# Kernel tuning notes

Measured on AMD Instinct MI355X. Metric: run time of the kernel, lower is better.

Reference implementation:

```python
import jax, jax.numpy as jnp
import numpy as np

EMBED = 1024
B, S = 4, 2048

def setup_inputs() -> dict:
    key = jax.random.key(0)
    k1, k2, k3, k4, k5, k6 = jax.random.split(key, 6)
    scale = 1.0 / np.sqrt(EMBED)
    return {
        "query": jax.random.normal(k1, (B, S, EMBED), dtype=jnp.float32),
        "key": jax.random.normal(k2, (B, S, EMBED), dtype=jnp.float32),
        "value": jax.random.normal(k3, (B, S, EMBED), dtype=jnp.float32),
        # nn.Linear weights, stored torch-style [out, in]; y = x @ W.T
        "Q_W": jax.random.normal(k4, (EMBED, EMBED), dtype=jnp.float32) * scale,
        "K_W": jax.random.normal(k5, (EMBED, EMBED), dtype=jnp.float32) * scale,
        "V_W": jax.random.normal(k6, (EMBED, EMBED), dtype=jnp.float32) * scale,
    }

def reference(query, key, value, Q_W, K_W, V_W):
    q = jnp.einsum('bse,oe->bso', query, Q_W)   # Linear(bias=False): x @ W.T
    k = jnp.einsum('bse,oe->bso', key, K_W)
    v = jnp.einsum('bse,oe->bso', value, V_W)
    scores = jnp.einsum('bqe,bke->bqk', q, k) / jnp.sqrt(jnp.asarray(q.shape[-1], q.dtype))
    attn = jax.nn.softmax(scores, axis=-1)      # [b, q, k]
    out = jnp.einsum('bqs,bse->bqe', attn, v)
    return out
```

## Files before the change

### kernel.cpp

```cpp
#include <hip/hip_runtime.h>
#include <stdint.h>


typedef __attribute__((ext_vector_type(8))) short short8;
typedef __attribute__((ext_vector_type(4))) float floatx4;
typedef __attribute__((ext_vector_type(4))) unsigned short u16x4;
typedef __attribute__((ext_vector_type(4))) float f32x4v;

__device__ __forceinline__ unsigned short f32_to_bf16(float f) {
    union { float f; unsigned u; } c; c.f = f;
    unsigned u = c.u;
    return (unsigned short)((u + 0x7fffu + ((u >> 16) & 1u)) >> 16);
}

#define G2L(g, l) __builtin_amdgcn_global_load_lds( \
    (__attribute__((address_space(1))) void*)(void*)(g), \
    (__attribute__((address_space(3))) void*)(l), 16, 0, 0)

#define BAR() __builtin_amdgcn_s_barrier()

#define MP_BLOCKS 256
#define CVT_BLOCKS 25608

__global__ __launch_bounds__(256) void cvt_all(
    const float* __restrict__ q, const float* __restrict__ k,
    const float* __restrict__ v, const float* __restrict__ wq,
    const float* __restrict__ wk, const float* __restrict__ wv,
    unsigned short* __restrict__ Xq, unsigned short* __restrict__ Xk,
    unsigned short* __restrict__ Xv, unsigned short* __restrict__ Wv,
    unsigned short* __restrict__ Mp, float* __restrict__ rowsum) {
    __shared__ float TtA[64][33];
    __shared__ float TtB[64][33];

    if (blockIdx.x < MP_BLOCKS) {
        const int id   = blockIdx.x;
        const int t0   = (id >> 4) * 64;
        const int k0   = (id & 15) * 64;
        const int tid  = threadIdx.x;
        const int lane = tid & 63;
        const int wave = tid >> 6;
        const int wm   = wave >> 1;
        const int wn   = wave & 1;
        const int lm   = lane & 15;
        const int quad = lane >> 4;
        const int r    = tid >> 3;
        const int c8   = (tid & 7) * 8;

        floatx4 acc[2][2];
#pragma unroll
        for (int i = 0; i < 2; ++i)
#pragma unroll
            for (int j = 0; j < 2; ++j) acc[i][j] = (floatx4)0.0f;

        for (int o0 = 0; o0 < 1024; o0 += 32) {
            const float* pa = &wk[(size_t)(o0 + r) * 1024 + t0 + c8];
            const float* pb = &wq[(size_t)(o0 + r) * 1024 + k0 + c8];
            const f32x4v a0 = *(const f32x4v*)pa;
            const f32x4v a1 = *(const f32x4v*)(pa + 4);
            const f32x4v b0 = *(const f32x4v*)pb;
            const f32x4v b1 = *(const f32x4v*)(pb + 4);
            __syncthreads();
#pragma unroll
            for (int j = 0; j < 4; ++j) {
                TtA[c8 + j][r]     = a0[j];
                TtA[c8 + 4 + j][r] = a1[j];
                TtB[c8 + j][r]     = b0[j];
                TtB[c8 + 4 + j][r] = b1[j];
            }
            __syncthreads();

            short8 aH[2], aL[2], bH[2], bL[2];
#pragma unroll
            for (int mt = 0; mt < 2; ++mt) {
                const int rowA = wm * 32 + mt * 16 + lm;
                const int rowB = wn * 32 + mt * 16 + lm;
#pragma unroll
                for (int e = 0; e < 8; ++e) {
                    const float fa = TtA[rowA][quad * 8 + e];
                    const unsigned short ha = f32_to_bf16(fa);
                    union { unsigned u; float f; } ca; ca.u = (unsigned)ha << 16;
                    aH[mt][e] = (short)ha;
                    aL[mt][e] = (short)f32_to_bf16(fa - ca.f);
                    const float fb = TtB[rowB][quad * 8 + e];
                    const unsigned short hb = f32_to_bf16(fb);
                    union { unsigned u; float f; } cb; cb.u = (unsigned)hb << 16;
                    bH[mt][e] = (short)hb;
                    bL[mt][e] = (short)f32_to_bf16(fb - cb.f);
                }
            }
#pragma unroll
            for (int mt = 0; mt < 2; ++mt)
#pragma unroll
                for (int nt = 0; nt < 2; ++nt) {
                    acc[mt][nt] = __builtin_amdgcn_mfma_f32_16x16x32_bf16(
                        aH[mt], bH[nt], acc[mt][nt], 0, 0, 0);
                    acc[mt][nt] = __builtin_amdgcn_mfma_f32_16x16x32_bf16(
                        aL[mt], bH[nt], acc[mt][nt], 0, 0, 0);
                    acc[mt][nt] = __builtin_amdgcn_mfma_f32_16x16x32_bf16(
                        aH[mt], bL[nt], acc[mt][nt], 0, 0, 0);
                }
        }
#pragma unroll
        for (int mt = 0; mt < 2; ++mt)
#pragma unroll
            for (int nt = 0; nt < 2; ++nt)
#pragma unroll
                for (int rr = 0; rr < 4; ++rr) {
                    const int row = t0 + wm * 32 + mt * 16 + quad * 4 + rr;
                    const int col = k0 + wn * 32 + nt * 16 + lm;
                    Mp[(size_t)row * 1024 + col] = f32_to_bf16(acc[mt][nt][rr]);
                }
        return;
    }

    const long NTE4 = 2097152;
    const long NW4  = 262144;
    long i = (long)(blockIdx.x - MP_BLOCKS) * 256 + threadIdx.x;
    const float* src;
    unsigned short* dst;
    long j;
    if (i < 3 * NTE4) {
        int a = (int)(i / NTE4); j = i - (long)a * NTE4;
        src = a == 0 ? q : a == 1 ? k : v;
        dst = a == 0 ? Xq : a == 1 ? Xk : Xv;
    } else {
        i -= 3 * NTE4;
        if (i < NW4) {
            src = wv; dst = Wv; j = i;
        } else {
            i -= NW4;
            if (i < 2048) ((f32x4v*)rowsum)[i] = (f32x4v)0.0f;
            return;
        }
    }
    f32x4v f = ((const f32x4v*)src)[j];
    u16x4 o;
#pragma unroll
    for (int t = 0; t < 4; ++t) o[t] = f32_to_bf16(f[t]);
    ((u16x4*)dst)[j] = o;
}

#define BM 128
#define BN 128
#define BK 64

template <int EPI>
__device__ __forceinline__ void gemm_body(
    const unsigned short* __restrict__ A, const unsigned short* __restrict__ B,
    void* __restrict__ Cv, int lda, int ldb, int ldc, int K, float scale,
    float* __restrict__ rowsum, int m0, int n0) {
    __shared__ unsigned short As[BM * BK];
    __shared__ unsigned short Bs[BN * BK];

    const int tid  = threadIdx.x;
    const int wave = tid >> 6;
    const int lane = tid & 63;
    const int lm   = lane & 15;
    const int quad = lane >> 4;
    const int wm   = wave >> 1;
    const int wn   = wave & 1;

    const int srow8 = lane >> 3;
    const int gcol  = ((lane & 7) ^ srow8) * 8;

    floatx4 acc[4][4];
#pragma unroll
    for (int i = 0; i < 4; ++i)
#pragma unroll
        for (int j = 0; j < 4; ++j) acc[i][j] = (floatx4)0.0f;

    for (int k0 = 0; k0 < K; k0 += BK) {
#pragma unroll
        for (int i = 0; i < 4; ++i) {
            const int rbase = wave * 32 + i * 8;
            G2L(A + (size_t)(m0 + rbase + srow8) * lda + k0 + gcol,
                &As[rbase * BK]);
            G2L(B + (size_t)(n0 + rbase + srow8) * ldb + k0 + gcol,
                &Bs[rbase * BK]);
        }
        __syncthreads();

#pragma unroll
        for (int s = 0; s < 2; ++s) {
            short8 af[4], bf[4];
#pragma unroll
            for (int t = 0; t < 4; ++t) {
                const int cs = ((s * 4 + quad) ^ (lm & 7)) * 8;
                af[t] = *(const short8*)&As[(wm * 64 + t * 16 + lm) * BK + cs];
                bf[t] = *(const short8*)&Bs[(wn * 64 + t * 16 + lm) * BK + cs];
            }
#pragma unroll
            for (int mt = 0; mt < 4; ++mt)
#pragma unroll
                for (int nt = 0; nt < 4; ++nt)
                    acc[mt][nt] = __builtin_amdgcn_mfma_f32_16x16x32_bf16(
                        af[mt], bf[nt], acc[mt][nt], 0, 0, 0);
        }
        __syncthreads();
    }

    if constexpr (EPI == 0) {
        unsigned short* C = (unsigned short*)Cv;
#pragma unroll
        for (int mt = 0; mt < 4; ++mt)
#pragma unroll
            for (int nt = 0; nt < 4; ++nt)
#pragma unroll
                for (int r = 0; r < 4; ++r) {
                    const int row = m0 + wm * 64 + mt * 16 + quad * 4 + r;
                    const int col = n0 + wn * 64 + nt * 16 + lm;
                    C[(size_t)row * ldc + col] = f32_to_bf16(acc[mt][nt][r]);
                }
    } else if constexpr (EPI == 2) {
        float* C = (float*)Cv;
#pragma unroll
        for (int mt = 0; mt < 4; ++mt)
#pragma unroll
            for (int r = 0; r < 4; ++r) {
                const int row = m0 + wm * 64 + mt * 16 + quad * 4 + r;
                const float inv = 1.0f / rowsum[row];
#pragma unroll
                for (int nt = 0; nt < 4; ++nt) {
                    const int col = n0 + wn * 64 + nt * 16 + lm;
                    C[(size_t)row * ldc + col] = acc[mt][nt][r] * inv;
                }
            }
    }
}

__global__ __launch_bounds__(256, 4) void proj_kernel(
    const unsigned short* __restrict__ Xq, const unsigned short* __restrict__ Mp,
    unsigned short* __restrict__ qb,
    const unsigned short* __restrict__ Wv, const unsigned short* __restrict__ Xv,
    unsigned short* __restrict__ vT) {
    const int z = blockIdx.z;
    const unsigned short* A = z == 0 ? Xq : Wv;
    const unsigned short* B = z == 0 ? Mp : Xv;
    unsigned short* C = z == 0 ? qb : vT;
    int m0, n0, ldc;
    if (z == 0) { m0 = blockIdx.x * BM; n0 = blockIdx.y * BN; ldc = 1024; }
    else        { m0 = blockIdx.y * BM; n0 = blockIdx.x * BN; ldc = 8192; }
    gemm_body<0>(A, B, C, 1024, 1024, ldc, 1024, 1.0f, nullptr, m0, n0);
}

__global__ __launch_bounds__(256, 4) void pv_kernel(
    const unsigned short* __restrict__ Sc, const unsigned short* __restrict__ vT,
    float* __restrict__ out, float* __restrict__ rowsum) {
    const long z = blockIdx.z;
    gemm_body<2>(Sc + z * 2048 * 2048, vT + z * 2048,
                 out + z * 2048 * 1024, 2048, 8192, 1024, 2048,
                 1.0f, rowsum + z * 2048,
                 blockIdx.x * BM, blockIdx.y * BN);
}

template <int EPI>
__device__ __forceinline__ void gemm256_body(
    const unsigned short* __restrict__ A, const unsigned short* __restrict__ B,
    void* __restrict__ Cv, int lda, int ldb, int ldc, int K, float scale,
    float* __restrict__ rowsum, int m0, int n0) {
    __shared__ unsigned short As[2][256 * 64];
    __shared__ unsigned short Bs[2][256 * 64];

    const int tid   = threadIdx.x;
    const int wave  = tid >> 6;
    const int lane  = tid & 63;
    const int lm    = lane & 15;
    const int quad  = lane >> 4;
    const int wm    = wave >> 2;
    const int wn    = wave & 3;
    const int srow8 = lane >> 3;
    const int gcol  = ((lane & 7) ^ srow8) * 8;
    const int KT    = K >> 6;

#define STAGE_A(buf, half, kcol) do { \
        const int r0_ = (half) * 128 + wave * 8; \
        G2L(A + (size_t)(m0 + r0_ + srow8) * lda + (kcol) + gcol, \
            &As[buf][r0_ * 64]); \
        G2L(A + (size_t)(m0 + r0_ + 64 + srow8) * lda + (kcol) + gcol, \
            &As[buf][(r0_ + 64) * 64]); \
    } while (0)
#define STAGE_B(buf, half, kcol) do { \
        const int r0_ = (half) * 128 + wave * 8; \
        G2L(B + (size_t)(n0 + r0_ + srow8) * ldb + (kcol) + gcol, \
            &Bs[buf][r0_ * 64]); \
        G2L(B + (size_t)(n0 + r0_ + 64 + srow8) * ldb + (kcol) + gcol, \
            &Bs[buf][(r0_ + 64) * 64]); \
    } while (0)

    floatx4 acc[8][4];
#pragma unroll
    for (int i = 0; i < 8; ++i)
#pragma unroll
        for (int j = 0; j < 4; ++j) acc[i][j] = (floatx4)0.0f;

    STAGE_A(0, 0, 0); STAGE_A(0, 1, 0); STAGE_B(0, 0, 0); STAGE_B(0, 1, 0);
    if (KT > 1) {
        STAGE_A(1, 0, 64); STAGE_A(1, 1, 64);
        STAGE_B(1, 0, 64); STAGE_B(1, 1, 64);
        asm volatile("s_waitcnt vmcnt(8)" ::: "memory");
    } else {
        asm volatile("s_waitcnt vmcnt(0)" ::: "memory");
    }
    BAR();

    short8 aA[2][4];
    short8 aM[2][4];
    short8 bB[2][2];

    for (int kt = 0; kt < KT; ++kt) {
        const int b = kt & 1;
        const unsigned short* Ab = As[b];
        const unsigned short* Bb = Bs[b];

#pragma unroll
        for (int s = 0; s < 2; ++s) {
            const int cs = ((s * 4 + quad) ^ (lm & 7)) * 8;
#pragma unroll
            for (int mt = 0; mt < 4; ++mt)
                aA[s][mt] = *(const short8*)&Ab[(wm * 128 + mt * 16 + lm) * 64 + cs];
#pragma unroll
            for (int nt = 0; nt < 2; ++nt)
                bB[s][nt] = *(const short8*)&Bb[(wn * 64 + nt * 16 + lm) * 64 + cs];
        }
#pragma unroll
        for (int s = 0; s < 2; ++s) {
            const int cs = ((s * 4 + quad) ^ (lm & 7)) * 8;
#pragma unroll
            for (int mt = 0; mt < 4; ++mt)
                aM[s][mt] = *(const short8*)&Ab[(wm * 128 + 64 + mt * 16 + lm) * 64 + cs];
        }
        BAR();
        __builtin_amdgcn_s_setprio(1);
#pragma unroll
        for (int s = 0; s < 2; ++s)
#pragma unroll
            for (int mt = 0; mt < 4; ++mt)
#pragma unroll
                for (int nt = 0; nt < 2; ++nt)
                    acc[mt][nt] = __builtin_amdgcn_mfma_f32_16x16x32_bf16(
                        aA[s][mt], bB[s][nt], acc[mt][nt], 0, 0, 0);
        __builtin_amdgcn_s_setprio(0);
        BAR();

        BAR();
        __builtin_amdgcn_s_setprio(1);
#pragma unroll
        for (int s = 0; s < 2; ++s)
#pragma unroll
            for (int mt = 0; mt < 4; ++mt)
#pragma unroll
                for (int nt = 0; nt < 2; ++nt)
                    acc[4 + mt][nt] = __builtin_amdgcn_mfma_f32_16x16x32_bf16(
                        aM[s][mt], bB[s][nt], acc[4 + mt][nt], 0, 0, 0);
        __builtin_amdgcn_s_setprio(0);
        BAR();

#pragma unroll
        for (int s = 0; s < 2; ++s) {
            const int cs = ((s * 4 + quad) ^ (lm & 7)) * 8;
#pragma unroll
            for (int nt = 0; nt < 2; ++nt)
                bB[s][nt] = *(const short8*)&Bb[(wn * 64 + 32 + nt * 16 + lm) * 64 + cs];
        }
        if (kt + 2 < KT) { STAGE_A(b, 0, (kt + 2) * 64); STAGE_A(b, 1, (kt + 2) * 64); }
        BAR();
        __builtin_amdgcn_s_setprio(1);
#pragma unroll
        for (int s = 0; s < 2; ++s)
#pragma unroll
            for (int mt = 0; mt < 4; ++mt)
#pragma unroll
                for (int nt = 0; nt < 2; ++nt)
                    acc[4 + mt][2 + nt] = __builtin_amdgcn_mfma_f32_16x16x32_bf16(
                        aM[s][mt], bB[s][nt], acc[4 + mt][2 + nt], 0, 0, 0);
        __builtin_amdgcn_s_setprio(0);
        BAR();

        if (kt + 2 < KT) { STAGE_B(b, 0, (kt + 2) * 64); STAGE_B(b, 1, (kt + 2) * 64); }
        BAR();
        __builtin_amdgcn_s_setprio(1);
#pragma unroll
        for (int s = 0; s < 2; ++s)
#pragma unroll
            for (int mt = 0; mt < 4; ++mt)
#pragma unroll
                for (int nt = 0; nt < 2; ++nt)
                    acc[mt][2 + nt] = __builtin_amdgcn_mfma_f32_16x16x32_bf16(
                        aA[s][mt], bB[s][nt], acc[mt][2 + nt], 0, 0, 0);
        __builtin_amdgcn_s_setprio(0);
        if (kt + 2 < KT) {
            asm volatile("s_waitcnt vmcnt(8)" ::: "memory");
        } else if (kt + 1 < KT) {
            asm volatile("s_waitcnt vmcnt(0)" ::: "memory");
        }
        BAR();
    }
#undef STAGE_A
#undef STAGE_B

    if constexpr (EPI == 1) {
        unsigned short* C = (unsigned short*)Cv;
        float psum[8][4];
#pragma unroll
        for (int f = 0; f < 8; ++f)
#pragma unroll
            for (int r = 0; r < 4; ++r) psum[f][r] = 0.0f;
#pragma unroll
        for (int f = 0; f < 8; ++f)
#pragma unroll
            for (int g = 0; g < 4; ++g)
#pragma unroll
                for (int r = 0; r < 4; ++r) {
                    const int row = m0 + wm * 128 + f * 16 + quad * 4 + r;
                    const int col = n0 + wn * 64 + g * 16 + lm;
                    const float p = __expf(acc[f][g][r] * scale);
                    psum[f][r] += p;
                    C[(size_t)row * ldc + col] = f32_to_bf16(p);
                }
#pragma unroll
        for (int off = 1; off <= 8; off <<= 1)
#pragma unroll
            for (int f = 0; f < 8; ++f)
#pragma unroll
                for (int r = 0; r < 4; ++r)
                    psum[f][r] += __shfl_xor(psum[f][r], off);
        if (lm == 0) {
#pragma unroll
            for (int f = 0; f < 8; ++f)
#pragma unroll
                for (int r = 0; r < 4; ++r)
                    atomicAdd(&rowsum[m0 + wm * 128 + f * 16 + quad * 4 + r],
                              psum[f][r]);
        }
    }
}

__global__ __launch_bounds__(512, 2) void scores256_kernel(
    const unsigned short* __restrict__ qb, const unsigned short* __restrict__ Xk,
    unsigned short* __restrict__ Sc, float* __restrict__ rowsum) {
    const long z = blockIdx.z;
    gemm256_body<1>(qb + z * 2048 * 1024, Xk + z * 2048 * 1024,
                    Sc + z * 2048 * 2048, 1024, 1024, 2048, 1024,
                    1.0f / 32.0f, rowsum + z * 2048,
                    blockIdx.x * 256, blockIdx.y * 256);
}

extern "C" void kernel_launch(void* const* d_in, const int* in_sizes, int n_in,
                              void* d_out, int out_size, void* d_ws, size_t ws_size,
                              hipStream_t stream) {
    const float* q_in = (const float*)d_in[0];
    const float* k_in = (const float*)d_in[1];
    const float* v_in = (const float*)d_in[2];
    const float* Qw_f = (const float*)d_in[3];
    const float* Kw_f = (const float*)d_in[4];
    const float* Vw_f = (const float*)d_in[5];
    float* out = (float*)d_out;

    const int Bb = 4, S = 2048, E = 1024;
    const size_t TOK = (size_t)Bb * S;
    const size_t NTE = TOK * E;
    const size_t NW  = (size_t)E * E;

    unsigned short* ws = (unsigned short*)d_ws;
    unsigned short* Xq = ws;
    unsigned short* Xk = Xq + NTE;
    unsigned short* Xv = Xk + NTE;
    unsigned short* Wv = Xv + NTE;
    unsigned short* Mp = Wv + NW;
    unsigned short* qb = Mp + NW;
    unsigned short* vT = qb + NTE;
    unsigned short* Sc = vT + NTE;
    float* rowsum = (float*)(Sc + (size_t)Bb * S * S);

    cvt_all<<<MP_BLOCKS + CVT_BLOCKS, 256, 0, stream>>>(
        q_in, k_in, v_in, Qw_f, Kw_f, Vw_f,
        Xq, Xk, Xv, Wv, Mp, rowsum);

    proj_kernel<<<dim3(TOK / BM, E / BN, 2), 256, 0, stream>>>(
        Xq, Mp, qb, Wv, Xv, vT);

    scores256_kernel<<<dim3(S / 256, S / 256, 4), 512, 0, stream>>>(
        qb, Xk, Sc, rowsum);

    pv_kernel<<<dim3(S / BM, E / BN, 4), 256, 0, stream>>>(
        Sc, vT, out, rowsum);
}
```

Measured before the change: 306.2 us.

## Split weight-product GEMM into its own kernel with register-prefetched 64-deep K tiles

```diff
diff --git a/kernel.cpp b/kernel.cpp
--- a/kernel.cpp
+++ b/kernel.cpp
@@ -19,56 +19,58 @@
 
 #define BAR() __builtin_amdgcn_s_barrier()
 
-#define MP_BLOCKS 256
-#define CVT_BLOCKS 25608
-
-__global__ __launch_bounds__(256) void cvt_all(
-    const float* __restrict__ q, const float* __restrict__ k,
-    const float* __restrict__ v, const float* __restrict__ wq,
-    const float* __restrict__ wk, const float* __restrict__ wv,
-    unsigned short* __restrict__ Xq, unsigned short* __restrict__ Xk,
-    unsigned short* __restrict__ Xv, unsigned short* __restrict__ Wv,
-    unsigned short* __restrict__ Mp, float* __restrict__ rowsum) {
-    __shared__ float TtA[64][33];
-    __shared__ float TtB[64][33];
-
-    if (blockIdx.x < MP_BLOCKS) {
-        const int id   = blockIdx.x;
-        const int t0   = (id >> 4) * 64;
-        const int k0   = (id & 15) * 64;
-        const int tid  = threadIdx.x;
-        const int lane = tid & 63;
-        const int wave = tid >> 6;
-        const int wm   = wave >> 1;
-        const int wn   = wave & 1;
-        const int lm   = lane & 15;
-        const int quad = lane >> 4;
-        const int r    = tid >> 3;
-        const int c8   = (tid & 7) * 8;
-
-        floatx4 acc[2][2];
-#pragma unroll
-        for (int i = 0; i < 2; ++i)
-#pragma unroll
-            for (int j = 0; j < 2; ++j) acc[i][j] = (floatx4)0.0f;
-
-        for (int o0 = 0; o0 < 1024; o0 += 32) {
-            const float* pa = &wk[(size_t)(o0 + r) * 1024 + t0 + c8];
-            const float* pb = &wq[(size_t)(o0 + r) * 1024 + k0 + c8];
-            const f32x4v a0 = *(const f32x4v*)pa;
-            const f32x4v a1 = *(const f32x4v*)(pa + 4);
-            const f32x4v b0 = *(const f32x4v*)pb;
-            const f32x4v b1 = *(const f32x4v*)(pb + 4);
-            __syncthreads();
+__global__ __launch_bounds__(256) void mp_kernel(
+    const float* __restrict__ wk, const float* __restrict__ wq,
+    unsigned short* __restrict__ Mp) {
+    __shared__ float TtA[64][65];
+    __shared__ float TtB[64][65];
+
+    const int t0   = ((int)blockIdx.x >> 4) * 64;
+    const int k0   = ((int)blockIdx.x & 15) * 64;
+    const int tid  = threadIdx.x;
+    const int lane = tid & 63;
+    const int wave = tid >> 6;
+    const int wm   = wave >> 1;
+    const int wn   = wave & 1;
+    const int lm   = lane & 15;
+    const int quad = lane >> 4;
+    const int r    = tid >> 2;
+    const int c4   = (tid & 3) * 16;
+
+    f32x4v av[4], bv[4];
+#pragma unroll
+    for (int p = 0; p < 4; ++p) {
+        av[p] = *(const f32x4v*)&wk[(size_t)r * 1024 + t0 + c4 + p * 4];
+        bv[p] = *(const f32x4v*)&wq[(size_t)r * 1024 + k0 + c4 + p * 4];
+    }
+
+    floatx4 acc[2][2];
+#pragma unroll
+    for (int i = 0; i < 2; ++i)
+#pragma unroll
+        for (int j = 0; j < 2; ++j) acc[i][j] = (floatx4)0.0f;
+
+    for (int o0 = 0; o0 < 1024; o0 += 64) {
+        if (o0) __syncthreads();
+#pragma unroll
+        for (int p = 0; p < 4; ++p)
 #pragma unroll
             for (int j = 0; j < 4; ++j) {
-                TtA[c8 + j][r]     = a0[j];
-                TtA[c8 + 4 + j][r] = a1[j];
-                TtB[c8 + j][r]     = b0[j];
-                TtB[c8 + 4 + j][r] = b1[j];
-            }
-            __syncthreads();
-
+                TtA[c4 + p * 4 + j][r] = av[p][j];
+                TtB[c4 + p * 4 + j][r] = bv[p][j];
+            }
+        __syncthreads();
+        if (o0 + 64 < 1024) {
+#pragma unroll
+            for (int p = 0; p < 4; ++p) {
+                av[p] = *(const f32x4v*)
+                    &wk[(size_t)(o0 + 64 + r) * 1024 + t0 + c4 + p * 4];
+                bv[p] = *(const f32x4v*)
+                    &wq[(size_t)(o0 + 64 + r) * 1024 + k0 + c4 + p * 4];
+            }
+        }
+#pragma unroll
+        for (int s = 0; s < 2; ++s) {
             short8 aH[2], aL[2], bH[2], bL[2];
 #pragma unroll
             for (int mt = 0; mt < 2; ++mt) {
@@ -76,12 +78,12 @@
                 const int rowB = wn * 32 + mt * 16 + lm;
 #pragma unroll
                 for (int e = 0; e < 8; ++e) {
-                    const float fa = TtA[rowA][quad * 8 + e];
+                    const float fa = TtA[rowA][s * 32 + quad * 8 + e];
                     const unsigned short ha = f32_to_bf16(fa);
                     union { unsigned u; float f; } ca; ca.u = (unsigned)ha << 16;
                     aH[mt][e] = (short)ha;
                     aL[mt][e] = (short)f32_to_bf16(fa - ca.f);
-                    const float fb = TtB[rowB][quad * 8 + e];
+                    const float fb = TtB[rowB][s * 32 + quad * 8 + e];
                     const unsigned short hb = f32_to_bf16(fb);
                     union { unsigned u; float f; } cb; cb.u = (unsigned)hb << 16;
                     bH[mt][e] = (short)hb;
@@ -100,22 +102,30 @@
                         aH[mt], bL[nt], acc[mt][nt], 0, 0, 0);
                 }
         }
-#pragma unroll
-        for (int mt = 0; mt < 2; ++mt)
-#pragma unroll
-            for (int nt = 0; nt < 2; ++nt)
-#pragma unroll
-                for (int rr = 0; rr < 4; ++rr) {
-                    const int row = t0 + wm * 32 + mt * 16 + quad * 4 + rr;
-                    const int col = k0 + wn * 32 + nt * 16 + lm;
-                    Mp[(size_t)row * 1024 + col] = f32_to_bf16(acc[mt][nt][rr]);
-                }
-        return;
-    }
-
+    }
+#pragma unroll
+    for (int mt = 0; mt < 2; ++mt)
+#pragma unroll
+        for (int nt = 0; nt < 2; ++nt)
+#pragma unroll
+            for (int rr = 0; rr < 4; ++rr) {
+                const int row = t0 + wm * 32 + mt * 16 + quad * 4 + rr;
+                const int col = k0 + wn * 32 + nt * 16 + lm;
+                Mp[(size_t)row * 1024 + col] = f32_to_bf16(acc[mt][nt][rr]);
+            }
+}
+
+#define CVT_BLOCKS 25608
+
+__global__ __launch_bounds__(256) void cvt_all(
+    const float* __restrict__ q, const float* __restrict__ k,
+    const float* __restrict__ v, const float* __restrict__ wv,
+    unsigned short* __restrict__ Xq, unsigned short* __restrict__ Xk,
+    unsigned short* __restrict__ Xv, unsigned short* __restrict__ Wv,
+    float* __restrict__ rowsum) {
     const long NTE4 = 2097152;
     const long NW4  = 262144;
-    long i = (long)(blockIdx.x - MP_BLOCKS) * 256 + threadIdx.x;
+    long i = (long)blockIdx.x * 256 + threadIdx.x;
     const float* src;
     unsigned short* dst;
     long j;
@@ -472,9 +482,10 @@
     unsigned short* Sc = vT + NTE;
     float* rowsum = (float*)(Sc + (size_t)Bb * S * S);
 
-    cvt_all<<<MP_BLOCKS + CVT_BLOCKS, 256, 0, stream>>>(
-        q_in, k_in, v_in, Qw_f, Kw_f, Vw_f,
-        Xq, Xk, Xv, Wv, Mp, rowsum);
+    mp_kernel<<<256, 256, 0, stream>>>(Kw_f, Qw_f, Mp);
+
+    cvt_all<<<CVT_BLOCKS, 256, 0, stream>>>(
+        q_in, k_in, v_in, Vw_f, Xq, Xk, Xv, Wv, rowsum);
 
     proj_kernel<<<dim3(TOK / BM, E / BN, 2), 256, 0, stream>>>(
         Xq, Mp, qb, Wv, Xv, vT);
```

New measurement: 298.0 us. 2.7% less time.
